# Kernel tuning notes

Hardware: AMD Instinct MI355X
Metric: run time of the kernel (lower is better)

Reference implementation:

```python
import jax, jax.numpy as jnp
import numpy as np

N, E, F, L, G, C = 100000, 1600000, 128, 3, 512, 40
BN_EPS = 1e-5


def gcn_conv(x, src, dst, W, b, n_nodes):
    # PyG GCNConv: linear transform, symmetric normalization with self-loops,
    # scatter-add aggregation, then bias.
    xw = x @ W                                   # [N, H]
    deg = jnp.zeros((n_nodes,), x.dtype).at[dst].add(1.0) + 1.0  # +1 self-loop
    dinv = jax.lax.rsqrt(deg)                    # D^{-1/2}
    norm = dinv[src] * dinv[dst]                 # [E]
    msg = xw[src] * norm[:, None]                # gather + scale, [E, H]
    agg = jnp.zeros_like(xw).at[dst].add(msg)    # scatter-add to destinations
    agg = agg + xw * (dinv * dinv)[:, None]      # self-loop contribution
    return agg + b


def setup_inputs() -> dict:
    key = jax.random.key(0)
    ks = jax.random.split(key, 6)
    x = jax.random.normal(ks[0], (N, F), dtype=jnp.float32)
    edge_index = jax.random.randint(ks[1], (2, E), 0, N, dtype=jnp.int64)
    batch = jnp.sort(jax.random.randint(ks[2], (N,), 0, G, dtype=jnp.int64))
    conv_w = jax.random.normal(ks[3], (L, F, F), dtype=jnp.float32) * 0.05
    conv_b = jnp.zeros((L, F), dtype=jnp.float32)
    bn_gamma = jnp.ones((L, F), dtype=jnp.float32)
    bn_beta = jnp.zeros((L, F), dtype=jnp.float32)
    bn_mean = jnp.zeros((L, F), dtype=jnp.float32)
    bn_var = jnp.ones((L, F), dtype=jnp.float32)
    lin_w = jax.random.normal(ks[4], (F, C), dtype=jnp.float32) * 0.05
    lin_b = jnp.zeros((C,), dtype=jnp.float32)
    return {"x": x, "edge_index": edge_index, "batch": batch,
            "conv_w": conv_w, "conv_b": conv_b,
            "bn_gamma": bn_gamma, "bn_beta": bn_beta,
            "bn_mean": bn_mean, "bn_var": bn_var,
            "lin_w": lin_w, "lin_b": lin_b}


def reference(x, edge_index, batch, conv_w, conv_b, bn_gamma, bn_beta,
              bn_mean, bn_var, lin_w, lin_b):
    src, dst = edge_index[0], edge_index[1]
    h = x
    # layers 0..L-2: conv -> BN(eval) -> ReLU (dropout is identity in eval)
    for i in range(L - 1):
        h = gcn_conv(h, src, dst, conv_w[i], conv_b[i], N)
        h = (h - bn_mean[i]) * (bn_gamma[i] * jax.lax.rsqrt(bn_var[i] + BN_EPS)) + bn_beta[i]
        h = jax.nn.relu(h)
    # last conv (no BN/ReLU)
    h = gcn_conv(h, src, dst, conv_w[L - 1], conv_b[L - 1], N)
    # global_mean_pool over graphs
    sums = jnp.zeros((G, F), h.dtype).at[batch].add(h)
    counts = jnp.zeros((G,), h.dtype).at[batch].add(1.0)
    pooled = sums / jnp.maximum(counts, 1.0)[:, None]   # [G, F]
    return pooled @ lin_w + lin_b                        # [G, C]
```

## Files before the change

### kernel.cpp

```cpp
#include <hip/hip_runtime.h>

#define Nn 100000
#define Ee 1600000
#define Ff 128
#define Gg 512
#define Cc 40
#define NCH 2048
#define CH  49

__global__ void prep_scales_k(const float* __restrict__ conv_b,
                              const float* __restrict__ gamma,
                              const float* __restrict__ beta,
                              const float* __restrict__ mean,
                              const float* __restrict__ var,
                              float* __restrict__ sc, float* __restrict__ sh)
{
    int i = blockIdx.x * blockDim.x + threadIdx.x;
    if (i >= 3 * Ff) return;
    float b = conv_b[i];
    if (i < 2 * Ff) {
        float s = gamma[i] * rsqrtf(var[i] + 1e-5f);
        sc[i] = s;
        sh[i] = (b - mean[i]) * s + beta[i];
    } else {
        sc[i] = 1.0f;
        sh[i] = b;
    }
}

__global__ void count_edges_k(const int* __restrict__ dst, int* __restrict__ deg)
{
    int e = blockIdx.x * 256 + threadIdx.x;
    if (e < Ee) atomicAdd(&deg[dst[e]], 1);
}

__global__ void chunk_sum_k(const int* __restrict__ deg, int* __restrict__ csum)
{
    int t = blockIdx.x * 256 + threadIdx.x;
    if (t >= NCH) return;
    int i0 = t * CH, i1 = min(i0 + CH, Nn);
    int s = 0;
    for (int i = i0; i < i1; ++i) s += deg[i];
    csum[t] = s;
}

__global__ void scan_chunks_k(const int* __restrict__ csum, int* __restrict__ coff)
{
    __shared__ int tot[256];
    int t = threadIdx.x;
    int v[8]; int s = 0;
    #pragma unroll
    for (int j = 0; j < 8; ++j) { v[j] = csum[t * 8 + j]; s += v[j]; }
    tot[t] = s;
    __syncthreads();
    for (int d = 1; d < 256; d <<= 1) {
        int x = (t >= d) ? tot[t - d] : 0;
        __syncthreads();
        tot[t] += x;
        __syncthreads();
    }
    int base = tot[t] - s;
    #pragma unroll
    for (int j = 0; j < 8; ++j) { coff[t * 8 + j] = base; base += v[j]; }
}

__global__ void write_offsets_k(const int* __restrict__ deg, const int* __restrict__ coff,
                                int* __restrict__ off, float* __restrict__ dinv)
{
    int t = blockIdx.x * 256 + threadIdx.x;
    if (t >= NCH) return;
    int i0 = t * CH, i1 = min(i0 + CH, Nn);
    int run = coff[t];
    for (int i = i0; i < i1; ++i) {
        off[i] = run;
        int d = deg[i];
        run += d;
        dinv[i] = rsqrtf((float)d + 1.0f);
    }
    if (t == 0) off[Nn] = Ee;
}

__global__ void fill_csr_k(const int* __restrict__ src, const int* __restrict__ dst,
                           const int* __restrict__ off, int* __restrict__ cur,
                           int* __restrict__ csrc)
{
    int e = blockIdx.x * 256 + threadIdx.x;
    if (e < Ee) {
        int d = dst[e];
        int p = off[d] + atomicAdd(&cur[d], 1);
        csrc[p] = src[e];
    }
}

__global__ __launch_bounds__(512) void gemm_scale_k(
    const float* __restrict__ A, const float* __restrict__ W,
    const float* __restrict__ dinv, float* __restrict__ Y, int n)
{
    __shared__ float Ws[Ff * Ff];
    __shared__ float As[Ff * Ff];
    const int tid = threadIdx.x;
    const int base = blockIdx.x * 128;

    {
        const float4* Wv = (const float4*)W;
        float4* Wsv = (float4*)Ws;
        #pragma unroll
        for (int i = 0; i < 8; ++i) Wsv[tid + i * 512] = Wv[tid + i * 512];
    }
    {
        #pragma unroll
        for (int i = 0; i < 8; ++i) {
            int idx = tid + i * 512;
            int r   = idx >> 5;
            int c4  = (idx & 31) << 2;
            int gr  = base + r;
            float4 v = make_float4(0.f, 0.f, 0.f, 0.f);
            if (gr < n) v = *(const float4*)(A + (size_t)gr * Ff + c4);
            int s = (r >> 2) & 31;
            As[r * Ff + ((c4 + 0) ^ s)] = v.x;
            As[r * Ff + ((c4 + 1) ^ s)] = v.y;
            As[r * Ff + ((c4 + 2) ^ s)] = v.z;
            As[r * Ff + ((c4 + 3) ^ s)] = v.w;
        }
    }
    __syncthreads();

    const int rg = tid & 31;
    const int cg = tid >> 5;
    float acc[4][8];
    #pragma unroll
    for (int a = 0; a < 4; ++a)
        #pragma unroll
        for (int b = 0; b < 8; ++b) acc[a][b] = 0.f;

    const float* pA0 = As + (rg * 4 + 0) * Ff;
    const float* pA1 = As + (rg * 4 + 1) * Ff;
    const float* pA2 = As + (rg * 4 + 2) * Ff;
    const float* pA3 = As + (rg * 4 + 3) * Ff;
    const float4* pW = ((const float4*)Ws) + (cg << 1);

    #pragma unroll 4
    for (int k = 0; k < 128; ++k) {
        const int kx = k ^ rg;
        const float a0 = pA0[kx], a1 = pA1[kx], a2 = pA2[kx], a3 = pA3[kx];
        const float4 w0 = pW[k * 32];
        const float4 w1 = pW[k * 32 + 1];
        const float wv[8] = {w0.x, w0.y, w0.z, w0.w, w1.x, w1.y, w1.z, w1.w};
        #pragma unroll
        for (int j = 0; j < 8; ++j) {
            acc[0][j] += a0 * wv[j];
            acc[1][j] += a1 * wv[j];
            acc[2][j] += a2 * wv[j];
            acc[3][j] += a3 * wv[j];
        }
    }

    #pragma unroll
    for (int jr = 0; jr < 4; ++jr) {
        int gr = base + rg * 4 + jr;
        if (gr < n) {
            float di = dinv[gr];
            float4 o0 = make_float4(acc[jr][0] * di, acc[jr][1] * di,
                                    acc[jr][2] * di, acc[jr][3] * di);
            float4 o1 = make_float4(acc[jr][4] * di, acc[jr][5] * di,
                                    acc[jr][6] * di, acc[jr][7] * di);
            *(float4*)(Y + (size_t)gr * Ff + cg * 8)     = o0;
            *(float4*)(Y + (size_t)gr * Ff + cg * 8 + 4) = o1;
        }
    }
}

__global__ __launch_bounds__(256) void aggregate_k(
    const float* __restrict__ Y, const int* __restrict__ off,
    const int* __restrict__ srcs, const float* __restrict__ dinv,
    const float* __restrict__ sc, const float* __restrict__ sh,
    float* __restrict__ H, int dorelu, int n)
{
    int wid  = threadIdx.x >> 6;
    int lane = threadIdx.x & 63;
    int node = blockIdx.x * 4 + wid;
    if (node >= n) return;
    int beg = off[node], end = off[node + 1];
    int c = lane * 2;

    float2 self = *(const float2*)(Y + (size_t)node * Ff + c);
    float ax = self.x, ay = self.y;
    float bx = 0.f,    by = 0.f;

    for (int e = beg; e < end; e += 64) {
        int nb = min(64, end - e);
        int sidx = (lane < nb) ? srcs[e + lane] : 0;
        int j = 0;
        for (; j + 4 <= nb; j += 4) {
            int s0 = __shfl(sidx, j);
            int s1 = __shfl(sidx, j + 1);
            int s2 = __shfl(sidx, j + 2);
            int s3 = __shfl(sidx, j + 3);
            float2 v0 = *(const float2*)(Y + (size_t)s0 * Ff + c);
            float2 v1 = *(const float2*)(Y + (size_t)s1 * Ff + c);
            float2 v2 = *(const float2*)(Y + (size_t)s2 * Ff + c);
            float2 v3 = *(const float2*)(Y + (size_t)s3 * Ff + c);
            ax += v0.x; ay += v0.y; bx += v1.x; by += v1.y;
            ax += v2.x; ay += v2.y; bx += v3.x; by += v3.y;
        }
        for (; j < nb; ++j) {
            int s0 = __shfl(sidx, j);
            float2 v0 = *(const float2*)(Y + (size_t)s0 * Ff + c);
            ax += v0.x; ay += v0.y;
        }
    }
    float di = dinv[node];
    float2 scv = *(const float2*)(sc + c);
    float2 shv = *(const float2*)(sh + c);
    float ox = (ax + bx) * di * scv.x + shv.x;
    float oy = (ay + by) * di * scv.y + shv.y;
    if (dorelu) { ox = fmaxf(ox, 0.f); oy = fmaxf(oy, 0.f); }
    *(float2*)(H + (size_t)node * Ff + c) = make_float2(ox, oy);
}

__global__ __launch_bounds__(128) void pool_linear_k(
    const float* __restrict__ H, const int* __restrict__ batch,
    const float* __restrict__ lw, const float* __restrict__ lb,
    float* __restrict__ out)
{
    int g = blockIdx.x, f = threadIdx.x;
    int lo = 0, hi = Nn;
    while (lo < hi) { int m = (lo + hi) >> 1; if (batch[m] < g) lo = m + 1; else hi = m; }
    int start = lo;
    hi = Nn;
    while (lo < hi) { int m = (lo + hi) >> 1; if (batch[m] < g + 1) lo = m + 1; else hi = m; }
    int end = lo;

    float a0 = 0.f, a1 = 0.f, a2 = 0.f, a3 = 0.f;
    int i = start;
    for (; i + 4 <= end; i += 4) {
        a0 += H[(size_t)(i + 0) * Ff + f];
        a1 += H[(size_t)(i + 1) * Ff + f];
        a2 += H[(size_t)(i + 2) * Ff + f];
        a3 += H[(size_t)(i + 3) * Ff + f];
    }
    for (; i < end; ++i) a0 += H[(size_t)i * Ff + f];
    int cnt = end - start;
    __shared__ float pooled[Ff];
    pooled[f] = ((a0 + a1) + (a2 + a3)) / (float)max(cnt, 1);
    __syncthreads();
    if (f < Cc) {
        float o = lb[f];
        #pragma unroll 8
        for (int k = 0; k < Ff; ++k) o += pooled[k] * lw[k * Cc + f];
        out[g * Cc + f] = o;
    }
}

extern "C" void kernel_launch(void* const* d_in, const int* in_sizes, int n_in,
                              void* d_out, int out_size, void* d_ws, size_t ws_size,
                              hipStream_t stream)
{
    const float* x      = (const float*)d_in[0];
    const int*   ei     = (const int*)d_in[1];
    const int*   batch  = (const int*)d_in[2];
    const float* conv_w = (const float*)d_in[3];
    const float* conv_b = (const float*)d_in[4];
    const float* gamma  = (const float*)d_in[5];
    const float* beta   = (const float*)d_in[6];
    const float* mean   = (const float*)d_in[7];
    const float* var    = (const float*)d_in[8];
    const float* lw     = (const float*)d_in[9];
    const float* lb     = (const float*)d_in[10];
    float* out = (float*)d_out;

    const int* srcp = ei;
    const int* dstp = ei + Ee;

    float* h    = (float*)d_ws;
    float* y    = h + (size_t)Nn * Ff;
    float* dinv = y + (size_t)Nn * Ff;
    float* sc   = dinv + Nn;
    float* sh   = sc + 3 * Ff;
    int*   deg  = (int*)(sh + 3 * Ff);
    int*   cur  = deg + Nn;
    int*   off  = cur + Nn;
    int*   csrc = off + (Nn + 1);
    int*   csum = csrc + Ee;
    int*   coff = csum + NCH;

    hipMemsetAsync(deg, 0, 2 * (size_t)Nn * sizeof(int), stream);

    prep_scales_k<<<2, 256, 0, stream>>>(conv_b, gamma, beta, mean, var, sc, sh);
    count_edges_k<<<Ee / 256, 256, 0, stream>>>(dstp, deg);
    chunk_sum_k<<<NCH / 256, 256, 0, stream>>>(deg, csum);
    scan_chunks_k<<<1, 256, 0, stream>>>(csum, coff);
    write_offsets_k<<<NCH / 256, 256, 0, stream>>>(deg, coff, off, dinv);
    fill_csr_k<<<Ee / 256, 256, 0, stream>>>(srcp, dstp, off, cur, csrc);

    const int gemm_grid = (Nn + 127) / 128;
    const int agg_grid  = (Nn + 3) / 4;
    for (int l = 0; l < 3; ++l) {
        const float* in = (l == 0) ? x : h;
        gemm_scale_k<<<gemm_grid, 512, 0, stream>>>(in, conv_w + (size_t)l * Ff * Ff,
                                                    dinv, y, Nn);
        aggregate_k<<<agg_grid, 256, 0, stream>>>(y, off, csrc, dinv,
                                                  sc + l * Ff, sh + l * Ff,
                                                  h, (l < 2) ? 1 : 0, Nn);
    }
    pool_linear_k<<<Gg, 128, 0, stream>>>(h, batch, lw, lb, out);
}
```

Measured before the change: 900.2 us.

## Rewrite GEMM without LDS staging and gather aggregation with half-wave float4 loads

The GEMM drops shared-memory staging of W and A. Each wave now owns 32 output columns and each lane computes two rows, reading A directly from global memory and W through wave-uniform scalar/cached loads, which removes LDS traffic and the block barrier. The aggregation kernel splits each wave into two halves that each gather a different neighbour row with float4 loads, then combines the halves with a cross-half shuffle. This doubles bytes per load and the number of edges in flight, at the cost of an extra reduction step and half the lanes sitting idle during the epilogue.

Result: faster. 858.7 us (-4.6%).

```diff
diff --git a/kernel.cpp b/kernel.cpp
--- a/kernel.cpp
+++ b/kernel.cpp
@@ -92,81 +92,56 @@
     }
 }
 
-__global__ __launch_bounds__(512) void gemm_scale_k(
+__global__ __launch_bounds__(256) void gemm_scale_k(
     const float* __restrict__ A, const float* __restrict__ W,
     const float* __restrict__ dinv, float* __restrict__ Y, int n)
 {
-    __shared__ float Ws[Ff * Ff];
-    __shared__ float As[Ff * Ff];
-    const int tid = threadIdx.x;
-    const int base = blockIdx.x * 128;
-
-    {
-        const float4* Wv = (const float4*)W;
-        float4* Wsv = (float4*)Ws;
+    const int lane = threadIdx.x & 63;
+    const int wv   = threadIdx.x >> 6;
+    const int colBase = __builtin_amdgcn_readfirstlane(wv) * 32;
+    const int r0 = blockIdx.x * 128 + lane;
+    const int r1 = r0 + 64;
+    const float* a0p = A + (size_t)min(r0, n - 1) * Ff;
+    const float* a1p = A + (size_t)min(r1, n - 1) * Ff;
+    const float* Wp  = W + colBase;
+
+    float acc0[32], acc1[32];
+    #pragma unroll
+    for (int c = 0; c < 32; ++c) { acc0[c] = 0.f; acc1[c] = 0.f; }
+
+    #pragma unroll 2
+    for (int k4 = 0; k4 < 32; ++k4) {
+        const float4 a0 = *(const float4*)(a0p + k4 * 4);
+        const float4 a1 = *(const float4*)(a1p + k4 * 4);
         #pragma unroll
-        for (int i = 0; i < 8; ++i) Wsv[tid + i * 512] = Wv[tid + i * 512];
-    }
-    {
+        for (int kk = 0; kk < 4; ++kk) {
+            const float* wr = Wp + (k4 * 4 + kk) * Ff;
+            const float av0 = (&a0.x)[kk];
+            const float av1 = (&a1.x)[kk];
+            #pragma unroll
+            for (int c = 0; c < 32; ++c) {
+                const float wvv = wr[c];
+                acc0[c] = fmaf(av0, wvv, acc0[c]);
+                acc1[c] = fmaf(av1, wvv, acc1[c]);
+            }
+        }
+    }
+
+    if (r0 < n) {
+        const float di = dinv[r0];
+        float* yp = Y + (size_t)r0 * Ff + colBase;
         #pragma unroll
-        for (int i = 0; i < 8; ++i) {
-            int idx = tid + i * 512;
-            int r   = idx >> 5;
-            int c4  = (idx & 31) << 2;
-            int gr  = base + r;
-            float4 v = make_float4(0.f, 0.f, 0.f, 0.f);
-            if (gr < n) v = *(const float4*)(A + (size_t)gr * Ff + c4);
-            int s = (r >> 2) & 31;
-            As[r * Ff + ((c4 + 0) ^ s)] = v.x;
-            As[r * Ff + ((c4 + 1) ^ s)] = v.y;
-            As[r * Ff + ((c4 + 2) ^ s)] = v.z;
-            As[r * Ff + ((c4 + 3) ^ s)] = v.w;
-        }
-    }
-    __syncthreads();
-
-    const int rg = tid & 31;
-    const int cg = tid >> 5;
-    float acc[4][8];
-    #pragma unroll
-    for (int a = 0; a < 4; ++a)
+        for (int c = 0; c < 32; c += 4)
+            *(float4*)(yp + c) = make_float4(acc0[c] * di, acc0[c + 1] * di,
+                                             acc0[c + 2] * di, acc0[c + 3] * di);
+    }
+    if (r1 < n) {
+        const float di = dinv[r1];
+        float* yp = Y + (size_t)r1 * Ff + colBase;
         #pragma unroll
-        for (int b = 0; b < 8; ++b) acc[a][b] = 0.f;
-
-    const float* pA0 = As + (rg * 4 + 0) * Ff;
-    const float* pA1 = As + (rg * 4 + 1) * Ff;
-    const float* pA2 = As + (rg * 4 + 2) * Ff;
-    const float* pA3 = As + (rg * 4 + 3) * Ff;
-    const float4* pW = ((const float4*)Ws) + (cg << 1);
-
-    #pragma unroll 4
-    for (int k = 0; k < 128; ++k) {
-        const int kx = k ^ rg;
-        const float a0 = pA0[kx], a1 = pA1[kx], a2 = pA2[kx], a3 = pA3[kx];
-        const float4 w0 = pW[k * 32];
-        const float4 w1 = pW[k * 32 + 1];
-        const float wv[8] = {w0.x, w0.y, w0.z, w0.w, w1.x, w1.y, w1.z, w1.w};
-        #pragma unroll
-        for (int j = 0; j < 8; ++j) {
-            acc[0][j] += a0 * wv[j];
-            acc[1][j] += a1 * wv[j];
-            acc[2][j] += a2 * wv[j];
-            acc[3][j] += a3 * wv[j];
-        }
-    }
-
-    #pragma unroll
-    for (int jr = 0; jr < 4; ++jr) {
-        int gr = base + rg * 4 + jr;
-        if (gr < n) {
-            float di = dinv[gr];
-            float4 o0 = make_float4(acc[jr][0] * di, acc[jr][1] * di,
-                                    acc[jr][2] * di, acc[jr][3] * di);
-            float4 o1 = make_float4(acc[jr][4] * di, acc[jr][5] * di,
-                                    acc[jr][6] * di, acc[jr][7] * di);
-            *(float4*)(Y + (size_t)gr * Ff + cg * 8)     = o0;
-            *(float4*)(Y + (size_t)gr * Ff + cg * 8 + 4) = o1;
-        }
+        for (int c = 0; c < 32; c += 4)
+            *(float4*)(yp + c) = make_float4(acc1[c] * di, acc1[c + 1] * di,
+                                             acc1[c + 2] * di, acc1[c + 3] * di);
     }
 }
 
@@ -176,46 +151,70 @@
     const float* __restrict__ sc, const float* __restrict__ sh,
     float* __restrict__ H, int dorelu, int n)
 {
-    int wid  = threadIdx.x >> 6;
-    int lane = threadIdx.x & 63;
-    int node = blockIdx.x * 4 + wid;
+    const int wid  = threadIdx.x >> 6;
+    const int lane = threadIdx.x & 63;
+    const int node = blockIdx.x * 4 + wid;
     if (node >= n) return;
-    int beg = off[node], end = off[node + 1];
-    int c = lane * 2;
-
-    float2 self = *(const float2*)(Y + (size_t)node * Ff + c);
-    float ax = self.x, ay = self.y;
-    float bx = 0.f,    by = 0.f;
+    const int beg = off[node], end = off[node + 1];
+    const int half = lane >> 5;
+    const int fl   = lane & 31;
+    const float4* Y4 = (const float4*)Y;
+
+    float ax = 0.f, ay = 0.f, az = 0.f, aw = 0.f;
+    float bx = 0.f, by = 0.f, bz = 0.f, bw = 0.f;
+    if (half == 0) {
+        float4 s4 = Y4[(size_t)node * 32 + fl];
+        ax = s4.x; ay = s4.y; az = s4.z; aw = s4.w;
+    }
 
     for (int e = beg; e < end; e += 64) {
-        int nb = min(64, end - e);
+        const int nb = min(64, end - e);
         int sidx = (lane < nb) ? srcs[e + lane] : 0;
         int j = 0;
-        for (; j + 4 <= nb; j += 4) {
-            int s0 = __shfl(sidx, j);
-            int s1 = __shfl(sidx, j + 1);
-            int s2 = __shfl(sidx, j + 2);
-            int s3 = __shfl(sidx, j + 3);
-            float2 v0 = *(const float2*)(Y + (size_t)s0 * Ff + c);
-            float2 v1 = *(const float2*)(Y + (size_t)s1 * Ff + c);
-            float2 v2 = *(const float2*)(Y + (size_t)s2 * Ff + c);
-            float2 v3 = *(const float2*)(Y + (size_t)s3 * Ff + c);
-            ax += v0.x; ay += v0.y; bx += v1.x; by += v1.y;
-            ax += v2.x; ay += v2.y; bx += v3.x; by += v3.y;
+        for (; j + 8 <= nb; j += 8) {
+            int s0 = __shfl(sidx, j + 0 + half);
+            int s1 = __shfl(sidx, j + 2 + half);
+            int s2 = __shfl(sidx, j + 4 + half);
+            int s3 = __shfl(sidx, j + 6 + half);
+            float4 v0 = Y4[(size_t)s0 * 32 + fl];
+            float4 v1 = Y4[(size_t)s1 * 32 + fl];
+            float4 v2 = Y4[(size_t)s2 * 32 + fl];
+            float4 v3 = Y4[(size_t)s3 * 32 + fl];
+            ax += v0.x; ay += v0.y; az += v0.z; aw += v0.w;
+            bx += v1.x; by += v1.y; bz += v1.z; bw += v1.w;
+            ax += v2.x; ay += v2.y; az += v2.z; aw += v2.w;
+            bx += v3.x; by += v3.y; bz += v3.z; bw += v3.w;
         }
-        for (; j < nb; ++j) {
-            int s0 = __shfl(sidx, j);
-            float2 v0 = *(const float2*)(Y + (size_t)s0 * Ff + c);
-            ax += v0.x; ay += v0.y;
+        for (; j < nb; j += 2) {
+            const int eo = j + half;
+            int s = __shfl(sidx, (eo < nb) ? eo : (nb - 1));
+            if (eo < nb) {
+                float4 v = Y4[(size_t)s * 32 + fl];
+                ax += v.x; ay += v.y; az += v.z; aw += v.w;
+            }
         }
     }
-    float di = dinv[node];
-    float2 scv = *(const float2*)(sc + c);
-    float2 shv = *(const float2*)(sh + c);
-    float ox = (ax + bx) * di * scv.x + shv.x;
-    float oy = (ay + by) * di * scv.y + shv.y;
-    if (dorelu) { ox = fmaxf(ox, 0.f); oy = fmaxf(oy, 0.f); }
-    *(float2*)(H + (size_t)node * Ff + c) = make_float2(ox, oy);
+    ax += bx; ay += by; az += bz; aw += bw;
+    float rx = ax + __shfl_xor(ax, 32);
+    float ry = ay + __shfl_xor(ay, 32);
+    float rz = az + __shfl_xor(az, 32);
+    float rw = aw + __shfl_xor(aw, 32);
+
+    if (half == 0) {
+        const float di = dinv[node];
+        const float4 scv = ((const float4*)sc)[fl];
+        const float4 shv = ((const float4*)sh)[fl];
+        float4 o;
+        o.x = rx * di * scv.x + shv.x;
+        o.y = ry * di * scv.y + shv.y;
+        o.z = rz * di * scv.z + shv.z;
+        o.w = rw * di * scv.w + shv.w;
+        if (dorelu) {
+            o.x = fmaxf(o.x, 0.f); o.y = fmaxf(o.y, 0.f);
+            o.z = fmaxf(o.z, 0.f); o.w = fmaxf(o.w, 0.f);
+        }
+        ((float4*)H)[(size_t)node * 32 + fl] = o;
+    }
 }
 
 __global__ __launch_bounds__(128) void pool_linear_k(
@@ -297,7 +296,7 @@
     const int agg_grid  = (Nn + 3) / 4;
     for (int l = 0; l < 3; ++l) {
         const float* in = (l == 0) ? x : h;
-        gemm_scale_k<<<gemm_grid, 512, 0, stream>>>(in, conv_w + (size_t)l * Ff * Ff,
+        gemm_scale_k<<<gemm_grid, 256, 0, stream>>>(in, conv_w + (size_t)l * Ff * Ff,
                                                     dinv, y, Nn);
         aggregate_k<<<agg_grid, 256, 0, stream>>>(y, off, csrc, dinv,
                                                   sc + l * Ff, sh + l * Ff,
```
